# Kernel optimization log

Measured on AMD Instinct MI355X. Metric: run time of the kernel, lower is better.

The kernel has to match this reference:

```python
import jax, jax.numpy as jnp
import numpy as np

B, S, D = 8, 512, 1024
F = 4 * D        # FFN hidden
E = 8            # num experts
SCALE = 0.02


def setup_inputs() -> dict:
    key = jax.random.key(0)
    ks = jax.random.split(key, 16)
    n = lambda k, shape, s=SCALE: (jax.random.normal(k, shape, dtype=jnp.float32) * s)
    task_ids = jax.random.randint(ks[15], (B,), 0, E)
    return {
        "hidden_states": jax.random.normal(ks[0], (B, S, D), dtype=jnp.float32),
        "ohe_task": jax.nn.one_hot(task_ids, E, dtype=jnp.float32),
        # base model (2-layer FFN) params
        "W1": n(ks[1], (D, F)), "b1": n(ks[2], (F,)),
        "W2": n(ks[3], (F, D)), "b2": n(ks[4], (D,)),
        # expert task vectors (expert_sd - base_sd), stacked over experts
        "T_W1": n(ks[5], (E, D, F)), "T_b1": n(ks[6], (E, F)),
        "T_W2": n(ks[7], (E, F, D)), "T_b2": n(ks[8], (E, D)),
        # gate: 2 hidden ReLU layers then linear to E
        "Wg1": n(ks[9], (D, D)), "bg1": jnp.zeros((D,), jnp.float32),
        "Wg2": n(ks[10], (D, D)), "bg2": jnp.zeros((D,), jnp.float32),
        "Wgo": n(ks[11], (D, E)), "bgo": jnp.zeros((E,), jnp.float32),
    }


def reference(hidden_states, ohe_task, W1, b1, W2, b2,
              T_W1, T_b1, T_W2, T_b2,
              Wg1, bg1, Wg2, bg2, Wgo, bgo):
    x = hidden_states  # [B,S,D]
    # --- router: per-token logits -> softmax over experts -> mean over seq ---
    h = jax.nn.relu(jnp.einsum("bsd,de->bse", x, Wg1) + bg1)
    h = jax.nn.relu(jnp.einsum("bsd,de->bse", h, Wg2) + bg2)
    logits = jnp.einsum("bsd,de->bse", h, Wgo) + bgo        # [B,S,E]
    gate_weights = jax.nn.softmax(logits, axis=-1).mean(axis=1)  # [B,E]
    # --- per-sample weighted merge of expert task vectors into base params ---
    coeff = gate_weights + ohe_task                          # [B,E]
    W1b = W1 + jnp.einsum("be,edf->bdf", coeff, T_W1)        # [B,D,F]
    b1b = b1 + coeff @ T_b1                                  # [B,F]
    W2b = W2 + jnp.einsum("be,efd->bfd", coeff, T_W2)        # [B,F,D]
    b2b = b2 + coeff @ T_b2                                  # [B,D]
    # --- batched functional forward through merged FFN ---
    hmid = jax.nn.gelu(jnp.einsum("bsd,bdf->bsf", x, W1b) + b1b[:, None, :],
                       approximate=False)
    out = jnp.einsum("bsf,bfd->bsd", hmid, W2b) + b2b[:, None, :]
    return out, gate_weights
```

## Files before the change

### kernel.cpp

```cpp
#include <hip/hip_runtime.h>
#include <hip/hip_bf16.h>

typedef __attribute__((ext_vector_type(8))) short s16x8;
typedef __attribute__((ext_vector_type(4))) float f32x4;

#define GLOAD_LDS16(gsrc, ldst) \
  __builtin_amdgcn_global_load_lds((const __attribute__((address_space(1))) void*)(gsrc), \
      (__attribute__((address_space(3))) void*)(ldst), 16, 0, 0)

__global__ __launch_bounds__(256) void cvt_bf16(const float* __restrict__ in,
                                                __hip_bfloat16* __restrict__ out, long n) {
  long i = ((long)blockIdx.x * 256 + threadIdx.x) * 4;
  if (i + 3 >= n) return;
  float4 v = *(const float4*)(in + i);
  __hip_bfloat16 tmp[4] = {__float2bfloat16(v.x), __float2bfloat16(v.y),
                           __float2bfloat16(v.z), __float2bfloat16(v.w)};
  *(ushort4*)((unsigned short*)out + i) = *(const ushort4*)tmp;
}

template<int NB>
__global__ __launch_bounds__(256) void merge_transpose(
    const float* __restrict__ Wb, const float* __restrict__ T,
    const float* __restrict__ coeff, __hip_bfloat16* __restrict__ Out,
    int K, int N, int nE) {
  int ntn = N >> 6;
  int k0 = (blockIdx.x / ntn) << 6;
  int n0 = (blockIdx.x % ntn) << 6;
  int t = threadIdx.x;
  long KN = (long)K * N;

  float accb[NB][16];
#pragma unroll
  for (int i = 0; i < 16; ++i) {
    int e = i * 256 + t; int kk = e >> 6, nn = e & 63;
    float bv = Wb[(long)(k0 + kk) * N + n0 + nn];
#pragma unroll
    for (int b2 = 0; b2 < NB; ++b2) accb[b2][i] = bv;
  }
  for (int ex = 0; ex < nE; ++ex) {
    float c[NB];
#pragma unroll
    for (int b2 = 0; b2 < NB; ++b2) c[b2] = coeff[b2 * 8 + ex];
#pragma unroll
    for (int i = 0; i < 16; ++i) {
      int e = i * 256 + t; int kk = e >> 6, nn = e & 63;
      float tv = T[(long)ex * KN + (long)(k0 + kk) * N + n0 + nn];
#pragma unroll
      for (int b2 = 0; b2 < NB; ++b2) accb[b2][i] += c[b2] * tv;
    }
  }
  __shared__ __hip_bfloat16 lds[64 * 66];
  for (int b2 = 0; b2 < NB; ++b2) {
    __syncthreads();
#pragma unroll
    for (int i = 0; i < 16; ++i) {
      int e = i * 256 + t; int kk = e >> 6, nn = e & 63;
      lds[kk * 66 + nn] = __float2bfloat16(accb[b2][i]);
    }
    __syncthreads();
#pragma unroll
    for (int i = 0; i < 16; ++i) {
      int o = i * 256 + t; int n2 = o >> 6, k2 = o & 63;
      Out[(long)b2 * KN + (long)(n0 + n2) * K + k0 + k2] = lds[k2 * 66 + n2];
    }
  }
}

__global__ __launch_bounds__(256) void merge_bias(const float* __restrict__ base,
                                                  const float* __restrict__ T,
                                                  const float* __restrict__ coeff,
                                                  float* __restrict__ out, int n) {
  int b = blockIdx.y;
  int i = blockIdx.x * 256 + threadIdx.x;
  if (i >= n) return;
  float v = base[i];
#pragma unroll
  for (int e = 0; e < 8; ++e) v += coeff[b * 8 + e] * T[(long)e * n + i];
  out[(long)b * n + i] = v;
}

template<int ACT, bool OUTBF>
__global__ __launch_bounds__(256, 2) void gemm_bt(
    const __hip_bfloat16* __restrict__ A, const __hip_bfloat16* __restrict__ BT,
    const float* __restrict__ bias, void* __restrict__ Out,
    int M, int N, int K, long sA, long sB, long sBias, long sOut) {
  int b = blockIdx.y;
  const __hip_bfloat16* Ab = A + (long)b * sA;
  const __hip_bfloat16* Bb = BT + (long)b * sB;
  const float* biasb = bias + (long)b * sBias;

  int ntn = N >> 7;
  int m0 = (blockIdx.x / ntn) << 7;
  int n0 = (blockIdx.x % ntn) << 7;

  __shared__ __align__(16) __hip_bfloat16 As[128 * 64];
  __shared__ __align__(16) __hip_bfloat16 Bs[128 * 64];

  int t = threadIdx.x;
  int lane = t & 63;
  int wid = t >> 6;
  int wm = wid >> 1, wn = wid & 1;
  int lr = lane & 15, kg = lane >> 4;

  f32x4 acc[4][4] = {};

  for (int kt = 0; kt < K; kt += 64) {
#pragma unroll
    for (int is = 0; is < 4; ++is) {
      int ci = is * 256 + t;
      int row = ci >> 3, cpos = ci & 7;
      int csrc = cpos ^ (row & 7);
      GLOAD_LDS16(Ab + (long)(m0 + row) * K + kt + csrc * 8, &As[ci * 8]);
      GLOAD_LDS16(Bb + (long)(n0 + row) * K + kt + csrc * 8, &Bs[ci * 8]);
    }
    __syncthreads();
#pragma unroll
    for (int ks = 0; ks < 2; ++ks) {
      s16x8 af[4], bfr[4];
#pragma unroll
      for (int m = 0; m < 4; ++m) {
        int row = wm * 64 + m * 16 + lr;
        int c = (ks * 4 + kg) ^ (row & 7);
        af[m] = *(const s16x8*)&As[row * 64 + c * 8];
      }
#pragma unroll
      for (int n = 0; n < 4; ++n) {
        int row = wn * 64 + n * 16 + lr;
        int c = (ks * 4 + kg) ^ (row & 7);
        bfr[n] = *(const s16x8*)&Bs[row * 64 + c * 8];
      }
#pragma unroll
      for (int m = 0; m < 4; ++m)
#pragma unroll
        for (int n = 0; n < 4; ++n)
          acc[m][n] = __builtin_amdgcn_mfma_f32_16x16x32_bf16(af[m], bfr[n], acc[m][n], 0, 0, 0);
    }
    __syncthreads();
  }

#pragma unroll
  for (int n = 0; n < 4; ++n) {
    int col = n0 + wn * 64 + n * 16 + lr;
    float bv = biasb[col];
#pragma unroll
    for (int m = 0; m < 4; ++m) {
      int row0 = m0 + wm * 64 + m * 16 + kg * 4;
#pragma unroll
      for (int j = 0; j < 4; ++j) {
        float v = acc[m][n][j] + bv;
        if (ACT == 1) v = fmaxf(v, 0.f);
        else if (ACT == 2) v = 0.5f * v * (1.f + erff(v * 0.70710678118f));
        long off = (long)b * sOut + (long)(row0 + j) * N + col;
        if (OUTBF) ((__hip_bfloat16*)Out)[off] = __float2bfloat16(v);
        else ((float*)Out)[off] = v;
      }
    }
  }
}

__global__ __launch_bounds__(256) void router_logits(
    const __hip_bfloat16* __restrict__ Hg2, const float* __restrict__ Wgo,
    const float* __restrict__ bgo, float* __restrict__ probs) {
  int r = blockIdx.x;
  int t = threadIdx.x;
  float acc[8] = {};
#pragma unroll
  for (int j = 0; j < 4; ++j) {
    int k = j * 256 + t;
    float h = __bfloat162float(Hg2[(long)r * 1024 + k]);
    const float4* wp = (const float4*)&Wgo[k * 8];
    float4 w0 = wp[0], w1 = wp[1];
    acc[0] += h * w0.x; acc[1] += h * w0.y; acc[2] += h * w0.z; acc[3] += h * w0.w;
    acc[4] += h * w1.x; acc[5] += h * w1.y; acc[6] += h * w1.z; acc[7] += h * w1.w;
  }
#pragma unroll
  for (int off = 32; off >= 1; off >>= 1)
#pragma unroll
    for (int e = 0; e < 8; ++e) acc[e] += __shfl_down(acc[e], off);
  __shared__ float lds[4][8];
  int wid = t >> 6, lane = t & 63;
  if (lane == 0)
#pragma unroll
    for (int e = 0; e < 8; ++e) lds[wid][e] = acc[e];
  __syncthreads();
  if (t == 0) {
    float lg[8];
#pragma unroll
    for (int e = 0; e < 8; ++e) lg[e] = lds[0][e] + lds[1][e] + lds[2][e] + lds[3][e] + bgo[e];
    float mx = lg[0];
#pragma unroll
    for (int e = 1; e < 8; ++e) mx = fmaxf(mx, lg[e]);
    float s = 0.f;
#pragma unroll
    for (int e = 0; e < 8; ++e) { lg[e] = __expf(lg[e] - mx); s += lg[e]; }
    float inv = 1.f / s;
#pragma unroll
    for (int e = 0; e < 8; ++e) probs[(long)r * 8 + e] = lg[e] * inv;
  }
}

__global__ __launch_bounds__(256) void router_mean(
    const float* __restrict__ probs, const float* __restrict__ ohe,
    float* __restrict__ gate_out, float* __restrict__ coeff) {
  int b = blockIdx.x;
  int t = threadIdx.x;
  int e = t & 7, sg = t >> 3;
  float s = 0.f;
#pragma unroll
  for (int j = 0; j < 16; ++j)
    s += probs[((long)b * 512 + sg + j * 32) * 8 + e];
  __shared__ float lds[256];
  lds[t] = s;
  __syncthreads();
  if (t < 8) {
    float tot = 0.f;
#pragma unroll
    for (int g = 0; g < 32; ++g) tot += lds[g * 8 + t];
    float gw = tot / 512.f;
    gate_out[b * 8 + t] = gw;
    coeff[b * 8 + t] = gw + ohe[b * 8 + t];
  }
}

extern "C" void kernel_launch(void* const* d_in, const int* in_sizes, int n_in,
                              void* d_out, int out_size, void* d_ws, size_t ws_size,
                              hipStream_t stream) {
  const float* x    = (const float*)d_in[0];
  const float* ohe  = (const float*)d_in[1];
  const float* W1   = (const float*)d_in[2];
  const float* b1   = (const float*)d_in[3];
  const float* W2   = (const float*)d_in[4];
  const float* b2   = (const float*)d_in[5];
  const float* T_W1 = (const float*)d_in[6];
  const float* T_b1 = (const float*)d_in[7];
  const float* T_W2 = (const float*)d_in[8];
  const float* T_b2 = (const float*)d_in[9];
  const float* Wg1  = (const float*)d_in[10];
  const float* bg1  = (const float*)d_in[11];
  const float* Wg2  = (const float*)d_in[12];
  const float* bg2  = (const float*)d_in[13];
  const float* Wgo  = (const float*)d_in[14];
  const float* bgo  = (const float*)d_in[15];
  float* out = (float*)d_out;
  float* gate_out = out + (long)8 * 512 * 1024;

  char* w = (char*)d_ws;
  __hip_bfloat16* xb   = (__hip_bfloat16*)(w);
  __hip_bfloat16* Wg1T = (__hip_bfloat16*)(w + 8388608);
  __hip_bfloat16* Wg2T = (__hip_bfloat16*)(w + 10485760);
  __hip_bfloat16* Hg1  = (__hip_bfloat16*)(w + 12582912);
  __hip_bfloat16* Hg2  = (__hip_bfloat16*)(w + 20971520);
  float*          probs= (float*)(w + 29360128);
  float*          coeff= (float*)(w + 29491200);
  float*          b1b  = (float*)(w + 29492224);
  float*          b2b  = (float*)(w + 29623296);
  __hip_bfloat16* hmid = (__hip_bfloat16*)(w + 29656064);
  __hip_bfloat16* Wb   = (__hip_bfloat16*)(w + 63210496);

  cvt_bf16<<<4096, 256, 0, stream>>>(x, xb, (long)8 * 512 * 1024);
  merge_transpose<1><<<16 * 16, 256, 0, stream>>>(Wg1, nullptr, nullptr, Wg1T, 1024, 1024, 0);
  merge_transpose<1><<<16 * 16, 256, 0, stream>>>(Wg2, nullptr, nullptr, Wg2T, 1024, 1024, 0);
  gemm_bt<1, true><<<dim3(32 * 8, 1), 256, 0, stream>>>(xb, Wg1T, bg1, Hg1,
      4096, 1024, 1024, 0, 0, 0, 0);
  gemm_bt<1, true><<<dim3(32 * 8, 1), 256, 0, stream>>>(Hg1, Wg2T, bg2, Hg2,
      4096, 1024, 1024, 0, 0, 0, 0);
  router_logits<<<4096, 256, 0, stream>>>(Hg2, Wgo, bgo, probs);
  router_mean<<<8, 256, 0, stream>>>(probs, ohe, gate_out, coeff);
  merge_bias<<<dim3(16, 8), 256, 0, stream>>>(b1, T_b1, coeff, b1b, 4096);
  merge_bias<<<dim3(4, 8), 256, 0, stream>>>(b2, T_b2, coeff, b2b, 1024);
  merge_transpose<8><<<16 * 64, 256, 0, stream>>>(W1, T_W1, coeff, Wb, 1024, 4096, 8);
  gemm_bt<2, true><<<dim3(4 * 32, 8), 256, 0, stream>>>(xb, Wb, b1b, hmid,
      512, 4096, 1024, (long)512 * 1024, (long)4096 * 1024, 4096, (long)512 * 4096);
  merge_transpose<8><<<64 * 16, 256, 0, stream>>>(W2, T_W2, coeff, Wb, 4096, 1024, 8);
  gemm_bt<0, false><<<dim3(4 * 8, 8), 256, 0, stream>>>(hmid, Wb, b2b, out,
      512, 1024, 4096, (long)512 * 4096, (long)4096 * 1024, 1024, (long)512 * 1024);
}
```

Measured before the change: 286.7 us.

## Double-buffer GEMM LDS tiles and vectorize merge-transpose loads and stores

```diff
diff --git a/kernel.cpp b/kernel.cpp
--- a/kernel.cpp
+++ b/kernel.cpp
@@ -29,11 +29,11 @@
   int t = threadIdx.x;
   long KN = (long)K * N;
 
-  float accb[NB][16];
-#pragma unroll
-  for (int i = 0; i < 16; ++i) {
-    int e = i * 256 + t; int kk = e >> 6, nn = e & 63;
-    float bv = Wb[(long)(k0 + kk) * N + n0 + nn];
+  float4 accb[NB][4];
+#pragma unroll
+  for (int i = 0; i < 4; ++i) {
+    int e = i * 256 + t; int kk = e >> 4, nn = (e & 15) << 2;
+    float4 bv = *(const float4*)&Wb[(long)(k0 + kk) * N + n0 + nn];
 #pragma unroll
     for (int b2 = 0; b2 < NB; ++b2) accb[b2][i] = bv;
   }
@@ -42,26 +42,36 @@
 #pragma unroll
     for (int b2 = 0; b2 < NB; ++b2) c[b2] = coeff[b2 * 8 + ex];
 #pragma unroll
-    for (int i = 0; i < 16; ++i) {
-      int e = i * 256 + t; int kk = e >> 6, nn = e & 63;
-      float tv = T[(long)ex * KN + (long)(k0 + kk) * N + n0 + nn];
-#pragma unroll
-      for (int b2 = 0; b2 < NB; ++b2) accb[b2][i] += c[b2] * tv;
+    for (int i = 0; i < 4; ++i) {
+      int e = i * 256 + t; int kk = e >> 4, nn = (e & 15) << 2;
+      float4 tv = *(const float4*)&T[(long)ex * KN + (long)(k0 + kk) * N + n0 + nn];
+#pragma unroll
+      for (int b2 = 0; b2 < NB; ++b2) {
+        accb[b2][i].x += c[b2] * tv.x; accb[b2][i].y += c[b2] * tv.y;
+        accb[b2][i].z += c[b2] * tv.z; accb[b2][i].w += c[b2] * tv.w;
+      }
     }
   }
   __shared__ __hip_bfloat16 lds[64 * 66];
   for (int b2 = 0; b2 < NB; ++b2) {
     __syncthreads();
 #pragma unroll
-    for (int i = 0; i < 16; ++i) {
-      int e = i * 256 + t; int kk = e >> 6, nn = e & 63;
-      lds[kk * 66 + nn] = __float2bfloat16(accb[b2][i]);
+    for (int i = 0; i < 4; ++i) {
+      int e = i * 256 + t; int kk = e >> 4, nn = (e & 15) << 2;
+      lds[kk * 66 + nn + 0] = __float2bfloat16(accb[b2][i].x);
+      lds[kk * 66 + nn + 1] = __float2bfloat16(accb[b2][i].y);
+      lds[kk * 66 + nn + 2] = __float2bfloat16(accb[b2][i].z);
+      lds[kk * 66 + nn + 3] = __float2bfloat16(accb[b2][i].w);
     }
     __syncthreads();
 #pragma unroll
-    for (int i = 0; i < 16; ++i) {
-      int o = i * 256 + t; int n2 = o >> 6, k2 = o & 63;
-      Out[(long)b2 * KN + (long)(n0 + n2) * K + k0 + k2] = lds[k2 * 66 + n2];
+    for (int i = 0; i < 4; ++i) {
+      int o = i * 256 + t; int n2 = o >> 4, k2 = (o & 15) << 2;
+      __hip_bfloat16 tmp[4];
+#pragma unroll
+      for (int j = 0; j < 4; ++j) tmp[j] = lds[(k2 + j) * 66 + n2];
+      *(ushort4*)((unsigned short*)&Out[(long)b2 * KN + (long)(n0 + n2) * K + k0 + k2]) =
+          *(const ushort4*)tmp;
     }
   }
 }
@@ -93,8 +103,8 @@
   int m0 = (blockIdx.x / ntn) << 7;
   int n0 = (blockIdx.x % ntn) << 7;
 
-  __shared__ __align__(16) __hip_bfloat16 As[128 * 64];
-  __shared__ __align__(16) __hip_bfloat16 Bs[128 * 64];
+  __shared__ __align__(16) __hip_bfloat16 As[2][128 * 64];
+  __shared__ __align__(16) __hip_bfloat16 Bs[2][128 * 64];
 
   int t = threadIdx.x;
   int lane = t & 63;
@@ -104,16 +114,19 @@
 
   f32x4 acc[4][4] = {};
 
-  for (int kt = 0; kt < K; kt += 64) {
+  auto stage = [&](int buf, int ktile) {
+    int kt = ktile << 6;
 #pragma unroll
     for (int is = 0; is < 4; ++is) {
       int ci = is * 256 + t;
       int row = ci >> 3, cpos = ci & 7;
       int csrc = cpos ^ (row & 7);
-      GLOAD_LDS16(Ab + (long)(m0 + row) * K + kt + csrc * 8, &As[ci * 8]);
-      GLOAD_LDS16(Bb + (long)(n0 + row) * K + kt + csrc * 8, &Bs[ci * 8]);
-    }
-    __syncthreads();
+      GLOAD_LDS16(Ab + (long)(m0 + row) * K + kt + csrc * 8, &As[buf][ci * 8]);
+      GLOAD_LDS16(Bb + (long)(n0 + row) * K + kt + csrc * 8, &Bs[buf][ci * 8]);
+    }
+  };
+
+  auto compute = [&](int buf) {
 #pragma unroll
     for (int ks = 0; ks < 2; ++ks) {
       s16x8 af[4], bfr[4];
@@ -121,13 +134,13 @@
       for (int m = 0; m < 4; ++m) {
         int row = wm * 64 + m * 16 + lr;
         int c = (ks * 4 + kg) ^ (row & 7);
-        af[m] = *(const s16x8*)&As[row * 64 + c * 8];
+        af[m] = *(const s16x8*)&As[buf][row * 64 + c * 8];
       }
 #pragma unroll
       for (int n = 0; n < 4; ++n) {
         int row = wn * 64 + n * 16 + lr;
         int c = (ks * 4 + kg) ^ (row & 7);
-        bfr[n] = *(const s16x8*)&Bs[row * 64 + c * 8];
+        bfr[n] = *(const s16x8*)&Bs[buf][row * 64 + c * 8];
       }
 #pragma unroll
       for (int m = 0; m < 4; ++m)
@@ -135,8 +148,17 @@
         for (int n = 0; n < 4; ++n)
           acc[m][n] = __builtin_amdgcn_mfma_f32_16x16x32_bf16(af[m], bfr[n], acc[m][n], 0, 0, 0);
     }
+  };
+
+  int nk = K >> 6;
+  stage(0, 0);
+  __syncthreads();
+  for (int it = 0; it < nk - 1; ++it) {
+    stage((it + 1) & 1, it + 1);
+    compute(it & 1);
     __syncthreads();
   }
+  compute((nk - 1) & 1);
 
 #pragma unroll
   for (int n = 0; n < 4; ++n) {
```

Measured after the change: 288.9 us. About the same (+0.8%).
